# Kernel tuning notes

Hardware: AMD Instinct MI355X
Metric: run time of the kernel (lower is better)

Reference implementation:

```python
import jax, jax.numpy as jnp
import numpy as np

N = 100000
E = 1600000
IN_C = 128
HID_C = 32
HEADS = 4
OUT_C = 64
NUM_CLASSES = 2
NUM_GRAPHS = 64
NEG_SLOPE = 0.2  # PyG GATConv default leaky_relu slope


def _segment_softmax(logits, seg, num_segments):
    # logits: [E, H], seg: [E] destination node ids
    m = jax.ops.segment_max(logits, seg, num_segments=num_segments)
    m = jnp.where(jnp.isfinite(m), m, 0.0)
    e = jnp.exp(logits - m[seg])
    s = jax.ops.segment_sum(e, seg, num_segments=num_segments)
    return e / (s[seg] + 1e-16)


def _gat_conv(x, src, dst, W, att_src, att_dst, bias, heads, ch, concat):
    n = x.shape[0]
    h = (x @ W).reshape(n, heads, ch)                 # [N, H, C]
    a_src = jnp.sum(h * att_src, axis=-1)             # [N, H]
    a_dst = jnp.sum(h * att_dst, axis=-1)             # [N, H]
    alpha = jax.nn.leaky_relu(a_src[src] + a_dst[dst], NEG_SLOPE)  # [E, H]
    alpha = _segment_softmax(alpha, dst, n)
    msg = h[src] * alpha[:, :, None]                  # [E, H, C]
    out = jax.ops.segment_sum(msg, dst, num_segments=n)  # [N, H, C]
    out = out.reshape(n, heads * ch) if concat else out.mean(axis=1)
    return out + bias


def setup_inputs() -> dict:
    key = jax.random.key(0)
    ks = jax.random.split(key, 12)
    x = jax.random.normal(ks[0], (N, IN_C), dtype=jnp.float32)
    edge_index = jax.random.randint(ks[1], (2, E), 0, N, dtype=jnp.int32)
    batch = jnp.sort(jax.random.randint(ks[2], (N,), 0, NUM_GRAPHS, dtype=jnp.int32))
    s1 = 1.0 / np.sqrt(IN_C)
    W1 = jax.random.uniform(ks[3], (IN_C, HEADS * HID_C), minval=-s1, maxval=s1, dtype=jnp.float32)
    att_src1 = jax.random.normal(ks[4], (HEADS, HID_C), dtype=jnp.float32) * 0.1
    att_dst1 = jax.random.normal(ks[5], (HEADS, HID_C), dtype=jnp.float32) * 0.1
    b1 = jnp.zeros((HEADS * HID_C,), dtype=jnp.float32)
    s2 = 1.0 / np.sqrt(HEADS * HID_C)
    W2 = jax.random.uniform(ks[6], (HEADS * HID_C, OUT_C), minval=-s2, maxval=s2, dtype=jnp.float32)
    att_src2 = jax.random.normal(ks[7], (1, OUT_C), dtype=jnp.float32) * 0.1
    att_dst2 = jax.random.normal(ks[8], (1, OUT_C), dtype=jnp.float32) * 0.1
    b2 = jnp.zeros((OUT_C,), dtype=jnp.float32)
    sc = 1.0 / np.sqrt(OUT_C)
    Wc = jax.random.uniform(ks[9], (OUT_C, NUM_CLASSES), minval=-sc, maxval=sc, dtype=jnp.float32)
    bc = jnp.zeros((NUM_CLASSES,), dtype=jnp.float32)
    return {"x": x, "edge_index": edge_index, "batch": batch,
            "W1": W1, "att_src1": att_src1, "att_dst1": att_dst1, "b1": b1,
            "W2": W2, "att_src2": att_src2, "att_dst2": att_dst2, "b2": b2,
            "Wc": Wc, "bc": bc}


def reference(x, edge_index, batch, W1, att_src1, att_dst1, b1,
              W2, att_src2, att_dst2, b2, Wc, bc):
    # PyG GATConv adds self-loops by default
    loops = jnp.arange(N, dtype=edge_index.dtype)
    src = jnp.concatenate([edge_index[0], loops])
    dst = jnp.concatenate([edge_index[1], loops])
    # eval mode: dropout is identity
    h = _gat_conv(x, src, dst, W1, att_src1, att_dst1, b1, HEADS, HID_C, True)
    h = jax.nn.elu(h)
    h = _gat_conv(h, src, dst, W2, att_src2, att_dst2, b2, 1, OUT_C, False)
    h = jax.nn.elu(h)
    # global mean pool over graphs
    sums = jax.ops.segment_sum(h, batch, num_segments=NUM_GRAPHS)
    cnts = jax.ops.segment_sum(jnp.ones((N, 1), h.dtype), batch, num_segments=NUM_GRAPHS)
    pooled = sums / jnp.maximum(cnts, 1.0)
    return pooled @ Wc + bc
```

## Files before the change

### kernel.cpp

```cpp
#include <hip/hip_runtime.h>
#include <math.h>


typedef __attribute__((ext_vector_type(8))) short bf16x8;
typedef __attribute__((ext_vector_type(4))) float f32x4;

__device__ __forceinline__ unsigned f2bf_rne(float x){
  unsigned u = __float_as_uint(x);
  return (u + 0x7fffu + ((u >> 16) & 1u)) >> 16;
}
__device__ __forceinline__ unsigned pk_bf2(float a, float b){
  return f2bf_rne(a) | (f2bf_rne(b) << 16);
}
__device__ __forceinline__ void unpack8(uint4 q, float* f){
  f[0] = __uint_as_float(q.x << 16);
  f[1] = __uint_as_float(q.x & 0xffff0000u);
  f[2] = __uint_as_float(q.y << 16);
  f[3] = __uint_as_float(q.y & 0xffff0000u);
  f[4] = __uint_as_float(q.z << 16);
  f[5] = __uint_as_float(q.z & 0xffff0000u);
  f[6] = __uint_as_float(q.w << 16);
  f[7] = __uint_as_float(q.w & 0xffff0000u);
}


#define CHUNKE 8192

__global__ __launch_bounds__(256) void k_bucketcount(
    const int* __restrict__ dst, int* __restrict__ bcnt, int e, int NB)
{
  __shared__ int hcnt[512];
  const int tid = threadIdx.x;
  for (int b = tid; b < 512; b += 256) hcnt[b] = 0;
  __syncthreads();
  const int lo = blockIdx.x * CHUNKE;
  const int hi = min(lo + CHUNKE, e);
  for (int i = lo + tid; i < hi; i += 256)
    atomicAdd(&hcnt[dst[i] >> 8], 1);
  __syncthreads();
  for (int b = tid; b < NB; b += 256)
    if (hcnt[b]) atomicAdd(&bcnt[b], hcnt[b]);
}

__global__ __launch_bounds__(512) void k_bucketscan(
    const int* __restrict__ bcnt, int* __restrict__ bbase,
    int* __restrict__ cur, int* __restrict__ off, int e, int n, int NB,
    const float* __restrict__ W1, const float* __restrict__ as1w,
    const float* __restrict__ ad1w,
    const float* __restrict__ W2, const float* __restrict__ as2w,
    const float* __restrict__ ad2w,
    unsigned short* __restrict__ wa1, unsigned short* __restrict__ wa2)
{
  const int t = threadIdx.x;

  if (blockIdx.x == 1){
    for (int i = t; i < 2048; i += 512) wa2[i] = 0;
    __syncthreads();
    {
      int k = t >> 2, j = t & 3;
      float ds = 0.f, dd = 0.f;
      for (int cc = 0; cc < 32; ++cc){
        float wv = W1[k * 128 + j * 32 + cc];
        ds = fmaf(wv, as1w[j * 32 + cc], ds);
        dd = fmaf(wv, ad1w[j * 32 + cc], dd);
      }
      unsigned hs_ = f2bf_rne(ds); float hsf = __uint_as_float(hs_ << 16);
      unsigned ls_ = f2bf_rne(ds - hsf);
      unsigned hd_ = f2bf_rne(dd); float hdf = __uint_as_float(hd_ << 16);
      unsigned ld_ = f2bf_rne(dd - hdf);
      wa1[(j     ) * 128 + k] = (unsigned short)hs_;
      wa1[(j + 4 ) * 128 + k] = (unsigned short)ls_;
      wa1[(j + 8 ) * 128 + k] = (unsigned short)hd_;
      wa1[(j + 12) * 128 + k] = (unsigned short)ld_;
    }
    if (t < 128){
      int k = t;
      float ds = 0.f, dd = 0.f;
      for (int cc = 0; cc < 64; ++cc){
        float wv = W2[k * 64 + cc];
        ds = fmaf(wv, as2w[cc], ds);
        dd = fmaf(wv, ad2w[cc], dd);
      }
      unsigned hs_ = f2bf_rne(ds); float hsf = __uint_as_float(hs_ << 16);
      unsigned ls_ = f2bf_rne(ds - hsf);
      unsigned hd_ = f2bf_rne(dd); float hdf = __uint_as_float(hd_ << 16);
      unsigned ld_ = f2bf_rne(dd - hdf);
      wa2[ 0 * 128 + k] = (unsigned short)hs_;
      wa2[ 4 * 128 + k] = (unsigned short)ls_;
      wa2[ 8 * 128 + k] = (unsigned short)hd_;
      wa2[12 * 128 + k] = (unsigned short)ld_;
    }
    return;
  }

  __shared__ int sh[512];
  int v = (t < NB) ? bcnt[t] : 0;
  sh[t] = v;
  __syncthreads();
  for (int o = 1; o < 512; o <<= 1){
    int x = (t >= o) ? sh[t - o] : 0;
    __syncthreads();
    sh[t] += x;
    __syncthreads();
  }
  if (t < NB){
    int excl = sh[t] - v;
    bbase[t] = excl;
    cur[t]   = excl;
  }
  if (t == 0) off[n] = e;
}

__global__ __launch_bounds__(256) void k_partition(
    const int* __restrict__ src, const int* __restrict__ dst,
    int* __restrict__ cur, unsigned* __restrict__ packed, int e, int NB)
{
  __shared__ unsigned       recs[CHUNKE];
  __shared__ unsigned short bkt[CHUNKE];
  __shared__ int hcnt[512];
  __shared__ int hoff[512];
  __shared__ int hbase[512];

  const int tid = threadIdx.x;
  const int lo  = blockIdx.x * CHUNKE;
  const int hi  = min(lo + CHUNKE, e);
  const int cnt = hi - lo;

  hcnt[tid] = 0; hcnt[tid + 256] = 0;
  __syncthreads();
  for (int i = lo + tid; i < hi; i += 256)
    atomicAdd(&hcnt[dst[i] >> 8], 1);
  __syncthreads();

  hoff[tid] = hcnt[tid]; hoff[tid + 256] = hcnt[tid + 256];
  __syncthreads();
  for (int o = 1; o < 512; o <<= 1){
    int x0 = (tid >= o)       ? hoff[tid - o]       : 0;
    int x1 = (tid + 256 >= o) ? hoff[tid + 256 - o] : 0;
    __syncthreads();
    hoff[tid] += x0; hoff[tid + 256] += x1;
    __syncthreads();
  }

  int c0 = hcnt[tid], c1 = hcnt[tid + 256];
  int e0 = hoff[tid] - c0, e1 = hoff[tid + 256] - c1;
  hbase[tid]       = c0 ? atomicAdd(&cur[tid], c0)       : 0;
  hbase[tid + 256] = c1 ? atomicAdd(&cur[tid + 256], c1) : 0;
  __syncthreads();
  hoff[tid] = e0; hoff[tid + 256] = e1;
  hcnt[tid] = 0;  hcnt[tid + 256] = 0;
  __syncthreads();

  for (int i = lo + tid; i < hi; i += 256){
    int d = dst[i];
    int b = d >> 8;
    int p = hoff[b] + atomicAdd(&hcnt[b], 1);
    recs[p] = (unsigned)src[i] | ((unsigned)(d & 255) << 17);
    bkt[p]  = (unsigned short)b;
  }
  __syncthreads();

  for (int t = tid; t < cnt; t += 256){
    int b = bkt[t];
    packed[hbase[b] + t - hoff[b]] = recs[t];
  }
}

__global__ __launch_bounds__(256) void k_bucketbuild(
    const unsigned* __restrict__ packed, const int* __restrict__ bbase,
    const int* __restrict__ bcnt, int* __restrict__ off,
    int* __restrict__ csr, int n)
{
  __shared__ int lcnt[256];
  __shared__ int loff[256];
  const int b    = blockIdx.x;
  const int tid  = threadIdx.x;
  const int seg0 = bbase[b];
  const int scnt = bcnt[b];

  lcnt[tid] = 0;
  __syncthreads();
  for (int i = tid; i < scnt; i += 256)
    atomicAdd(&lcnt[packed[seg0 + i] >> 17], 1);
  __syncthreads();
  int v = lcnt[tid];
  loff[tid] = v;
  __syncthreads();
  for (int o = 1; o < 256; o <<= 1){
    int x = (tid >= o) ? loff[tid - o] : 0;
    __syncthreads();
    loff[tid] += x;
    __syncthreads();
  }
  int excl = loff[tid] - v;
  __syncthreads();
  loff[tid] = excl;
  lcnt[tid] = 0;
  int d = (b << 8) + tid;
  if (d < n) off[d] = seg0 + excl;
  __syncthreads();
  for (int i = tid; i < scnt; i += 256){
    unsigned rec = packed[seg0 + i];
    int doff = rec >> 17;
    int s    = rec & 0x1FFFF;
    int p    = atomicAdd(&lcnt[doff], 1);
    csr[seg0 + loff[doff] + p] = s;
  }
}


template<int OUTC, int HEADS, bool XBF16, typename XT>
__global__ __launch_bounds__(256) void k_gemm_mfma(
    const XT* __restrict__ X, const float* __restrict__ W,
    const unsigned short* __restrict__ WATT,
    unsigned short* __restrict__ H, float* __restrict__ ASRC,
    float* __restrict__ ADST, int n)
{
  constexpr int K  = 128;
  constexpr int KC = 32;
  constexpr int CT = OUTC / 16;
  constexpr int CTX = CT + 1;
  constexpr int RT = 16 / CT;
  constexpr int WROWS = RT * 16;
  constexpr int BROWS = WROWS * 4;

  __shared__ unsigned short Bs[OUTC + 16][K + 8];
  __shared__ unsigned short As[BROWS][KC + 8];

  const int tid   = threadIdx.x;
  const int lane  = tid & 63;
  const int c15   = lane & 15;
  const int quad  = lane >> 4;
  const int warow = (tid >> 6) * WROWS;
  const int row0  = blockIdx.x * BROWS;

  f32x4 acc[CTX][RT];
  #pragma unroll
  for (int ct = 0; ct < CTX; ++ct)
    #pragma unroll
    for (int t = 0; t < RT; ++t)
      #pragma unroll
      for (int r = 0; r < 4; ++r) acc[ct][t][r] = 0.f;

  for (int idx = tid; idx < K * OUTC / 4; idx += 256){
    int k  = idx / (OUTC / 4);
    int c4 = (idx % (OUTC / 4)) * 4;
    float4 v = *(const float4*)&W[(size_t)k * OUTC + c4];
    Bs[c4 + 0][k] = (unsigned short)f2bf_rne(v.x);
    Bs[c4 + 1][k] = (unsigned short)f2bf_rne(v.y);
    Bs[c4 + 2][k] = (unsigned short)f2bf_rne(v.z);
    Bs[c4 + 3][k] = (unsigned short)f2bf_rne(v.w);
  }
  for (int idx = tid; idx < 16 * (K / 8); idx += 256){
    int rr = idx >> 4;
    int q  = idx & 15;
    *(uint4*)&Bs[OUTC + rr][q * 8] = *(const uint4*)&WATT[rr * K + q * 8];
  }

  for (int kc = 0; kc < K; kc += KC){
    if (XBF16){
      for (int idx = tid; idx < BROWS * (KC / 8); idx += 256){
        int rr = idx / (KC / 8);
        int q  = idx % (KC / 8);
        int row = row0 + rr;
        uint4 v = make_uint4(0, 0, 0, 0);
        if (row < n) v = *(const uint4*)((const unsigned short*)X + (size_t)row * K + kc + q * 8);
        *(uint4*)&As[rr][q * 8] = v;
      }
    } else {
      for (int idx = tid; idx < BROWS * (KC / 4); idx += 256){
        int rr = idx / (KC / 4);
        int q  = idx % (KC / 4);
        int row = row0 + rr;
        float4 v = make_float4(0.f, 0.f, 0.f, 0.f);
        if (row < n) v = *(const float4*)((const float*)X + (size_t)row * K + kc + q * 4);
        *(uint2*)&As[rr][q * 4] = make_uint2(pk_bf2(v.x, v.y), pk_bf2(v.z, v.w));
      }
    }
    __syncthreads();

    bf16x8 af[RT];
    #pragma unroll
    for (int t = 0; t < RT; ++t)
      af[t] = *(const bf16x8*)&As[warow + t * 16 + c15][8 * quad];
    #pragma unroll
    for (int ct = 0; ct < CTX; ++ct){
      bf16x8 bfr = *(const bf16x8*)&Bs[ct * 16 + c15][kc + 8 * quad];
      #pragma unroll
      for (int t = 0; t < RT; ++t)
        acc[ct][t] = __builtin_amdgcn_mfma_f32_16x16x32_bf16(af[t], bfr, acc[ct][t], 0, 0, 0);
    }
    __syncthreads();
  }

  #pragma unroll
  for (int t = 0; t < RT; ++t){
    #pragma unroll
    for (int r = 0; r < 4; ++r){
      int row = row0 + warow + t * 16 + quad * 4 + r;
      float av = acc[CT][t][r];
      av += __shfl_xor(av, 4);
      if (row < n){
        #pragma unroll
        for (int ct = 0; ct < CT; ++ct)
          H[(size_t)row * OUTC + ct * 16 + c15] = (unsigned short)f2bf_rne(acc[ct][t][r]);
        if (c15 < HEADS)                      ASRC[row * HEADS + c15] = av;
        else if (c15 >= 8 && c15 < 8 + HEADS) ADST[row * HEADS + c15 - 8] = av;
      }
    }
  }
}


template<int CH, int HEADS, bool OUTBF16, bool POOL>
__global__ __launch_bounds__(256) void k_aggregate(
    const unsigned short* __restrict__ Hmsg, const float* __restrict__ ASRC,
    const float* __restrict__ ADST, const int* __restrict__ off,
    const int* __restrict__ csr, const float* __restrict__ bias,
    void* __restrict__ OUT, const int* __restrict__ batch,
    float* __restrict__ gsums, int n)
{
  constexpr int CL  = CH / 8;
  constexpr int GPB = 256 / CL;
  constexpr int CPH = CH / HEADS;
  constexpr int RQ  = CH / 8;

  __shared__ float lsum[POOL ? 256 : 1];

  const int tid = threadIdx.x;
  const int cl  = tid % CL;
  const int c0  = cl * 8;
  const int h   = c0 / CPH;
  const int d   = (int)blockIdx.x * GPB + tid / CL;
  const uint4* Hv = (const uint4*)Hmsg;

  int gbase = 0;
  if (POOL){
    int probe = (int)blockIdx.x * GPB;
    gbase = batch[probe < n - 1 ? probe : n - 1];
    lsum[tid] = 0.f;
    __syncthreads();
  }

  if (d < n){
    const float adst = ADST[d * HEADS + h];

    float acc[8];
    float wsum;
    {
      float t = ASRC[d * HEADS + h] + adst;
      float w = __expf(fmaxf(t, 0.2f * t));
      float f[8];
      unpack8(Hv[d * RQ + cl], f);
      #pragma unroll
      for (int j = 0; j < 8; ++j) acc[j] = w * f[j];
      wsum = w;
    }

    const int s0   = off[d];
    const int cnt  = off[d + 1] - s0;
    const int full = cnt & ~7;

    for (int p = 0; p < full; p += 8){
      int idx[8];
      #pragma unroll
      for (int j = 0; j < 8; ++j) idx[j] = csr[s0 + p + j];
      float av[8];
      #pragma unroll
      for (int j = 0; j < 8; ++j) av[j] = ASRC[idx[j] * HEADS + h];
      uint4 hq[8];
      #pragma unroll
      for (int j = 0; j < 8; ++j) hq[j] = Hv[idx[j] * RQ + cl];
      #pragma unroll
      for (int j = 0; j < 8; ++j){
        float t = av[j] + adst;
        float w = __expf(fmaxf(t, 0.2f * t));
        float f[8];
        unpack8(hq[j], f);
        #pragma unroll
        for (int q = 0; q < 8; ++q) acc[q] = fmaf(w, f[q], acc[q]);
        wsum += w;
      }
    }

    const int rem = cnt - full;
    if (rem){
      int  idx[8];
      bool ok[8];
      #pragma unroll
      for (int j = 0; j < 8; ++j){
        int q = csr[s0 + full + j];
        ok[j]  = j < rem;
        idx[j] = ok[j] ? q : 0;
      }
      float av[8];
      #pragma unroll
      for (int j = 0; j < 8; ++j) av[j] = ASRC[idx[j] * HEADS + h];
      uint4 hq[8];
      #pragma unroll
      for (int j = 0; j < 8; ++j) hq[j] = Hv[idx[j] * RQ + cl];
      #pragma unroll
      for (int j = 0; j < 8; ++j){
        float t = av[j] + adst;
        float w = __expf(fmaxf(t, 0.2f * t));
        w = ok[j] ? w : 0.f;
        float f[8];
        unpack8(hq[j], f);
        #pragma unroll
        for (int q = 0; q < 8; ++q) acc[q] = fmaf(w, f[q], acc[q]);
        wsum += w;
      }
    }

    const float inv = 1.f / (wsum + 1e-16f);
    float o[8];
    #pragma unroll
    for (int j = 0; j < 8; ++j){
      float v = acc[j] * inv + bias[c0 + j];
      o[j] = v > 0.f ? v : expm1f(v);
    }
    if (POOL){
      int gb  = batch[d];
      int rel = gb - gbase;
      if (rel >= 0 && rel < 4){
        #pragma unroll
        for (int j = 0; j < 8; ++j) atomicAdd(&lsum[rel * 64 + c0 + j], o[j]);
      } else {
        #pragma unroll
        for (int j = 0; j < 8; ++j) atomicAdd(&gsums[gb * 64 + c0 + j], o[j]);
      }
    } else if (OUTBF16){
      uint4 q;
      q.x = pk_bf2(o[0], o[1]); q.y = pk_bf2(o[2], o[3]);
      q.z = pk_bf2(o[4], o[5]); q.w = pk_bf2(o[6], o[7]);
      *(uint4*)((unsigned short*)OUT + (size_t)d * CH + c0) = q;
    } else {
      float* Of = (float*)OUT;
      *(float4*)&Of[(size_t)d * CH + c0 + 0] = make_float4(o[0], o[1], o[2], o[3]);
      *(float4*)&Of[(size_t)d * CH + c0 + 4] = make_float4(o[4], o[5], o[6], o[7]);
    }
  }

  if (POOL){
    __syncthreads();
    int slot = tid >> 6;
    int ch   = tid & 63;
    float v = lsum[slot * 64 + ch];
    int gg = gbase + slot;
    if (v != 0.f && gg < 64)
      atomicAdd(&gsums[gg * 64 + ch], v);
  }
}

__global__ __launch_bounds__(128) void k_classify(
    const float* __restrict__ sums, const int* __restrict__ batch,
    const float* __restrict__ Wc, const float* __restrict__ bc,
    float* __restrict__ out, int n)
{
  int t = threadIdx.x;
  if (t >= 128) return;
  int g = t >> 1, cls = t & 1;
  int lo = 0, hi = n;
  while (lo < hi){ int m = (lo + hi) >> 1; if (batch[m] < g) lo = m + 1; else hi = m; }
  int s = lo;
  lo = s; hi = n;
  while (lo < hi){ int m = (lo + hi) >> 1; if (batch[m] < g + 1) lo = m + 1; else hi = m; }
  int cnt = lo - s;
  float inv = 1.f / (float)(cnt > 1 ? cnt : 1);
  float dot = 0.f;
  #pragma unroll
  for (int c = 0; c < 64; ++c) dot = fmaf(sums[g * 64 + c], Wc[c * 2 + cls], dot);
  out[g * 2 + cls] = dot * inv + bc[cls];
}


extern "C" void kernel_launch(void* const* d_in, const int* in_sizes, int n_in,
                              void* d_out, int out_size, void* d_ws, size_t ws_size,
                              hipStream_t stream)
{
  const float* x    = (const float*)d_in[0];
  const int*   edge = (const int*)  d_in[1];
  const int*   batch= (const int*)  d_in[2];
  const float* W1   = (const float*)d_in[3];
  const float* as1w = (const float*)d_in[4];
  const float* ad1w = (const float*)d_in[5];
  const float* b1   = (const float*)d_in[6];
  const float* W2   = (const float*)d_in[7];
  const float* as2w = (const float*)d_in[8];
  const float* ad2w = (const float*)d_in[9];
  const float* b2   = (const float*)d_in[10];
  const float* Wc   = (const float*)d_in[11];
  const float* bc   = (const float*)d_in[12];

  const int n = in_sizes[2];
  const int e = in_sizes[1] / 2;
  const int* esrc = edge;
  const int* edst = edge + e;
  const int NB = (n + 255) >> 8;

  unsigned short* h1  = (unsigned short*)d_ws;
  unsigned short* h1a = h1 + (size_t)n * 128;
  float* as1 = (float*)(h1a + (size_t)n * 128);
  float* ad1 = as1 + (size_t)n * 4;
  float* as2 = ad1 + (size_t)n * 4;
  float* ad2 = as2 + (size_t)n;
  float* sums = ad2 + (size_t)n;
  unsigned short* wa1 = (unsigned short*)(sums + 64 * 64);
  unsigned short* wa2 = wa1 + 2048;
  int*  bcnt  = (int*)(wa2 + 2048);
  int*  cur   = bcnt + 512;
  int*  bbase = cur + 512;
  int*  off   = bbase + 512;
  unsigned* packed = (unsigned*)(off + n + 1);
  int*  csr   = (int*)(packed + e);

  const int eb = (e + CHUNKE - 1) / CHUNKE;

  (void)hipMemsetAsync(sums, 0, 64 * 64 * 4 + 2 * 4096 + 512 * 4, stream);
  k_bucketcount<<<eb, 256, 0, stream>>>(edst, bcnt, e, NB);
  k_bucketscan <<<2, 512, 0, stream>>>(bcnt, bbase, cur, off, e, n, NB,
                                       W1, as1w, ad1w, W2, as2w, ad2w, wa1, wa2);
  k_partition  <<<eb, 256, 0, stream>>>(esrc, edst, cur, packed, e, NB);
  k_bucketbuild<<<NB, 256, 0, stream>>>(packed, bbase, bcnt, off, csr, n);

  k_gemm_mfma<128, 4, false><<<(n + 127) / 128, 256, 0, stream>>>(
      x, W1, wa1, h1, as1, ad1, n);
  k_aggregate<128, 4, true, false><<<(n + 15) / 16, 256, 0, stream>>>(
      h1, as1, ad1, off, csr, b1, (void*)h1a, nullptr, nullptr, n);

  unsigned short* h2 = h1;
  k_gemm_mfma<64, 1, true><<<(n + 255) / 256, 256, 0, stream>>>(
      h1a, W2, wa2, h2, as2, ad2, n);
  k_aggregate<64, 1, false, true><<<(n + 31) / 32, 256, 0, stream>>>(
      h2, as2, ad2, off, csr, b2, nullptr, batch, sums, n);

  k_classify<<<1, 128, 0, stream>>>(sums, batch, Wc, bc, (float*)d_out, n);
}
```

Measured before the change: 380.0 us.

## Fuse layer-2 GEMM into layer-1 aggregation and wave-reduce pooled atomics

```diff
diff --git a/kernel.cpp b/kernel.cpp
--- a/kernel.cpp
+++ b/kernel.cpp
@@ -49,12 +49,12 @@
     const float* __restrict__ ad1w,
     const float* __restrict__ W2, const float* __restrict__ as2w,
     const float* __restrict__ ad2w,
-    unsigned short* __restrict__ wa1, unsigned short* __restrict__ wa2)
+    unsigned short* __restrict__ wa1, unsigned short* __restrict__ w2b)
 {
   const int t = threadIdx.x;
 
   if (blockIdx.x == 1){
-    for (int i = t; i < 2048; i += 512) wa2[i] = 0;
+    for (int i = t; i < 16 * 128; i += 512) w2b[64 * 128 + i] = 0;
     __syncthreads();
     {
       int k = t >> 2, j = t & 3;
@@ -73,6 +73,10 @@
       wa1[(j + 8 ) * 128 + k] = (unsigned short)hd_;
       wa1[(j + 12) * 128 + k] = (unsigned short)ld_;
     }
+    for (int idx = t; idx < 64 * 128; idx += 512){
+      int col = idx & 63, k = idx >> 6;
+      w2b[col * 128 + k] = (unsigned short)f2bf_rne(W2[k * 64 + col]);
+    }
     if (t < 128){
       int k = t;
       float ds = 0.f, dd = 0.f;
@@ -85,10 +89,10 @@
       unsigned ls_ = f2bf_rne(ds - hsf);
       unsigned hd_ = f2bf_rne(dd); float hdf = __uint_as_float(hd_ << 16);
       unsigned ld_ = f2bf_rne(dd - hdf);
-      wa2[ 0 * 128 + k] = (unsigned short)hs_;
-      wa2[ 4 * 128 + k] = (unsigned short)ls_;
-      wa2[ 8 * 128 + k] = (unsigned short)hd_;
-      wa2[12 * 128 + k] = (unsigned short)ld_;
+      w2b[(64 +  0) * 128 + k] = (unsigned short)hs_;
+      w2b[(64 +  4) * 128 + k] = (unsigned short)ls_;
+      w2b[(64 +  8) * 128 + k] = (unsigned short)hd_;
+      w2b[(64 + 12) * 128 + k] = (unsigned short)ld_;
     }
     return;
   }
@@ -312,46 +316,41 @@
 }
 
 
-template<int CH, int HEADS, bool OUTBF16, bool POOL>
-__global__ __launch_bounds__(256) void k_aggregate(
+__global__ __launch_bounds__(256) void k_agg1_fused(
     const unsigned short* __restrict__ Hmsg, const float* __restrict__ ASRC,
     const float* __restrict__ ADST, const int* __restrict__ off,
     const int* __restrict__ csr, const float* __restrict__ bias,
-    void* __restrict__ OUT, const int* __restrict__ batch,
-    float* __restrict__ gsums, int n)
-{
-  constexpr int CL  = CH / 8;
-  constexpr int GPB = 256 / CL;
-  constexpr int CPH = CH / HEADS;
-  constexpr int RQ  = CH / 8;
-
-  __shared__ float lsum[POOL ? 256 : 1];
+    const unsigned short* __restrict__ W2b,
+    unsigned short* __restrict__ H2, float* __restrict__ AS2,
+    float* __restrict__ AD2, int n)
+{
+  __shared__ unsigned short Ht[16][136];
+  __shared__ unsigned short Bs2[80][136];
 
   const int tid = threadIdx.x;
-  const int cl  = tid % CL;
+  const int cl  = tid & 15;
   const int c0  = cl * 8;
-  const int h   = c0 / CPH;
-  const int d   = (int)blockIdx.x * GPB + tid / CL;
+  const int h   = cl >> 2;
+  const int ld  = tid >> 4;
+  const int d0  = (int)blockIdx.x * 16;
+  const int d   = d0 + ld;
   const uint4* Hv = (const uint4*)Hmsg;
 
-  int gbase = 0;
-  if (POOL){
-    int probe = (int)blockIdx.x * GPB;
-    gbase = batch[probe < n - 1 ? probe : n - 1];
-    lsum[tid] = 0.f;
-    __syncthreads();
+  for (int idx = tid; idx < 80 * 16; idx += 256){
+    int row = idx >> 4, q = idx & 15;
+    *(uint4*)&Bs2[row][q * 8] = *(const uint4*)&W2b[row * 128 + q * 8];
   }
 
   if (d < n){
-    const float adst = ADST[d * HEADS + h];
+    const float adst = ADST[d * 4 + h];
 
     float acc[8];
     float wsum;
     {
-      float t = ASRC[d * HEADS + h] + adst;
+      float t = ASRC[d * 4 + h] + adst;
       float w = __expf(fmaxf(t, 0.2f * t));
       float f[8];
-      unpack8(Hv[d * RQ + cl], f);
+      unpack8(Hv[d * 16 + cl], f);
       #pragma unroll
       for (int j = 0; j < 8; ++j) acc[j] = w * f[j];
       wsum = w;
@@ -367,10 +366,10 @@
       for (int j = 0; j < 8; ++j) idx[j] = csr[s0 + p + j];
       float av[8];
       #pragma unroll
-      for (int j = 0; j < 8; ++j) av[j] = ASRC[idx[j] * HEADS + h];
+      for (int j = 0; j < 8; ++j) av[j] = ASRC[idx[j] * 4 + h];
       uint4 hq[8];
       #pragma unroll
-      for (int j = 0; j < 8; ++j) hq[j] = Hv[idx[j] * RQ + cl];
+      for (int j = 0; j < 8; ++j) hq[j] = Hv[idx[j] * 16 + cl];
       #pragma unroll
       for (int j = 0; j < 8; ++j){
         float t = av[j] + adst;
@@ -395,10 +394,10 @@
       }
       float av[8];
       #pragma unroll
-      for (int j = 0; j < 8; ++j) av[j] = ASRC[idx[j] * HEADS + h];
+      for (int j = 0; j < 8; ++j) av[j] = ASRC[idx[j] * 4 + h];
       uint4 hq[8];
       #pragma unroll
-      for (int j = 0; j < 8; ++j) hq[j] = Hv[idx[j] * RQ + cl];
+      for (int j = 0; j < 8; ++j) hq[j] = Hv[idx[j] * 16 + cl];
       #pragma unroll
       for (int j = 0; j < 8; ++j){
         float t = av[j] + adst;
@@ -419,37 +418,195 @@
       float v = acc[j] * inv + bias[c0 + j];
       o[j] = v > 0.f ? v : expm1f(v);
     }
-    if (POOL){
-      int gb  = batch[d];
-      int rel = gb - gbase;
+    uint4 q;
+    q.x = pk_bf2(o[0], o[1]); q.y = pk_bf2(o[2], o[3]);
+    q.z = pk_bf2(o[4], o[5]); q.w = pk_bf2(o[6], o[7]);
+    *(uint4*)&Ht[ld][c0] = q;
+  }
+
+  __syncthreads();
+
+  const int lane = tid & 63;
+  const int c15  = lane & 15;
+  const int quad = lane >> 4;
+  const int w    = tid >> 6;
+  f32x4 a0, a4;
+  #pragma unroll
+  for (int r = 0; r < 4; ++r){ a0[r] = 0.f; a4[r] = 0.f; }
+
+  #pragma unroll
+  for (int kc = 0; kc < 128; kc += 32){
+    bf16x8 af = *(const bf16x8*)&Ht[c15][kc + 8 * quad];
+    bf16x8 b0 = *(const bf16x8*)&Bs2[w * 16 + c15][kc + 8 * quad];
+    a0 = __builtin_amdgcn_mfma_f32_16x16x32_bf16(af, b0, a0, 0, 0, 0);
+    if (w == 0){
+      bf16x8 b4 = *(const bf16x8*)&Bs2[64 + c15][kc + 8 * quad];
+      a4 = __builtin_amdgcn_mfma_f32_16x16x32_bf16(af, b4, a4, 0, 0, 0);
+    }
+  }
+
+  #pragma unroll
+  for (int r = 0; r < 4; ++r){
+    int dd = d0 + quad * 4 + r;
+    if (dd < n) H2[(size_t)dd * 64 + w * 16 + c15] = (unsigned short)f2bf_rne(a0[r]);
+  }
+  if (w == 0){
+    #pragma unroll
+    for (int r = 0; r < 4; ++r){
+      float av = a4[r] + __shfl_xor(a4[r], 4);
+      int dd = d0 + quad * 4 + r;
+      if (dd < n){
+        if (c15 == 0)      AS2[dd] = av;
+        else if (c15 == 8) AD2[dd] = av;
+      }
+    }
+  }
+}
+
+
+template<int CH, int HEADS>
+__global__ __launch_bounds__(256) void k_agg2_pool(
+    const unsigned short* __restrict__ Hmsg, const float* __restrict__ ASRC,
+    const float* __restrict__ ADST, const int* __restrict__ off,
+    const int* __restrict__ csr, const float* __restrict__ bias,
+    const int* __restrict__ batch, float* __restrict__ gsums, int n)
+{
+  constexpr int CL  = CH / 8;
+  constexpr int GPB = 256 / CL;
+  constexpr int RQ  = CH / 8;
+
+  __shared__ float lsum[256];
+
+  const int tid = threadIdx.x;
+  const int cl  = tid % CL;
+  const int c0  = cl * 8;
+  const int d   = (int)blockIdx.x * GPB + tid / CL;
+  const uint4* Hv = (const uint4*)Hmsg;
+
+  int probe = (int)blockIdx.x * GPB;
+  const int gbase = batch[probe < n - 1 ? probe : n - 1];
+  lsum[tid] = 0.f;
+  __syncthreads();
+
+  float o[8];
+  #pragma unroll
+  for (int j = 0; j < 8; ++j) o[j] = 0.f;
+  int gb = gbase;
+
+  if (d < n){
+    gb = batch[d];
+    const float adst = ADST[d];
+
+    float acc[8];
+    float wsum;
+    {
+      float t = ASRC[d] + adst;
+      float w = __expf(fmaxf(t, 0.2f * t));
+      float f[8];
+      unpack8(Hv[d * RQ + cl], f);
+      #pragma unroll
+      for (int j = 0; j < 8; ++j) acc[j] = w * f[j];
+      wsum = w;
+    }
+
+    const int s0   = off[d];
+    const int cnt  = off[d + 1] - s0;
+    const int full = cnt & ~7;
+
+    for (int p = 0; p < full; p += 8){
+      int idx[8];
+      #pragma unroll
+      for (int j = 0; j < 8; ++j) idx[j] = csr[s0 + p + j];
+      float av[8];
+      #pragma unroll
+      for (int j = 0; j < 8; ++j) av[j] = ASRC[idx[j]];
+      uint4 hq[8];
+      #pragma unroll
+      for (int j = 0; j < 8; ++j) hq[j] = Hv[idx[j] * RQ + cl];
+      #pragma unroll
+      for (int j = 0; j < 8; ++j){
+        float t = av[j] + adst;
+        float w = __expf(fmaxf(t, 0.2f * t));
+        float f[8];
+        unpack8(hq[j], f);
+        #pragma unroll
+        for (int q = 0; q < 8; ++q) acc[q] = fmaf(w, f[q], acc[q]);
+        wsum += w;
+      }
+    }
+
+    const int rem = cnt - full;
+    if (rem){
+      int  idx[8];
+      bool ok[8];
+      #pragma unroll
+      for (int j = 0; j < 8; ++j){
+        int q = csr[s0 + full + j];
+        ok[j]  = j < rem;
+        idx[j] = ok[j] ? q : 0;
+      }
+      float av[8];
+      #pragma unroll
+      for (int j = 0; j < 8; ++j) av[j] = ASRC[idx[j]];
+      uint4 hq[8];
+      #pragma unroll
+      for (int j = 0; j < 8; ++j) hq[j] = Hv[idx[j] * RQ + cl];
+      #pragma unroll
+      for (int j = 0; j < 8; ++j){
+        float t = av[j] + adst;
+        float w = __expf(fmaxf(t, 0.2f * t));
+        w = ok[j] ? w : 0.f;
+        float f[8];
+        unpack8(hq[j], f);
+        #pragma unroll
+        for (int q = 0; q < 8; ++q) acc[q] = fmaf(w, f[q], acc[q]);
+        wsum += w;
+      }
+    }
+
+    const float inv = 1.f / (wsum + 1e-16f);
+    #pragma unroll
+    for (int j = 0; j < 8; ++j){
+      float v = acc[j] * inv + bias[c0 + j];
+      o[j] = v > 0.f ? v : expm1f(v);
+    }
+  }
+
+  int gb0 = __shfl(gb, 0, 64);
+  bool uni = __all(gb == gb0);
+  if (uni){
+    #pragma unroll
+    for (int s = CL; s < 64; s <<= 1)
+      #pragma unroll
+      for (int j = 0; j < 8; ++j) o[j] += __shfl_xor(o[j], s);
+    if ((tid & 63) < CL){
+      int rel = gb0 - gbase;
       if (rel >= 0 && rel < 4){
         #pragma unroll
         for (int j = 0; j < 8; ++j) atomicAdd(&lsum[rel * 64 + c0 + j], o[j]);
       } else {
         #pragma unroll
-        for (int j = 0; j < 8; ++j) atomicAdd(&gsums[gb * 64 + c0 + j], o[j]);
-      }
-    } else if (OUTBF16){
-      uint4 q;
-      q.x = pk_bf2(o[0], o[1]); q.y = pk_bf2(o[2], o[3]);
-      q.z = pk_bf2(o[4], o[5]); q.w = pk_bf2(o[6], o[7]);
-      *(uint4*)((unsigned short*)OUT + (size_t)d * CH + c0) = q;
+        for (int j = 0; j < 8; ++j) atomicAdd(&gsums[gb0 * 64 + c0 + j], o[j]);
+      }
+    }
+  } else if (d < n){
+    int rel = gb - gbase;
+    if (rel >= 0 && rel < 4){
+      #pragma unroll
+      for (int j = 0; j < 8; ++j) atomicAdd(&lsum[rel * 64 + c0 + j], o[j]);
     } else {
-      float* Of = (float*)OUT;
-      *(float4*)&Of[(size_t)d * CH + c0 + 0] = make_float4(o[0], o[1], o[2], o[3]);
-      *(float4*)&Of[(size_t)d * CH + c0 + 4] = make_float4(o[4], o[5], o[6], o[7]);
-    }
-  }
-
-  if (POOL){
-    __syncthreads();
-    int slot = tid >> 6;
-    int ch   = tid & 63;
-    float v = lsum[slot * 64 + ch];
-    int gg = gbase + slot;
-    if (v != 0.f && gg < 64)
-      atomicAdd(&gsums[gg * 64 + ch], v);
-  }
+      #pragma unroll
+      for (int j = 0; j < 8; ++j) atomicAdd(&gsums[gb * 64 + c0 + j], o[j]);
+    }
+  }
+
+  __syncthreads();
+  int slot = tid >> 6;
+  int ch   = tid & 63;
+  float v = lsum[slot * 64 + ch];
+  int gg = gbase + slot;
+  if (v != 0.f && gg < 64)
+    atomicAdd(&gsums[gg * 64 + ch], v);
 }
 
 __global__ __launch_bounds__(128) void k_classify(
@@ -499,15 +656,15 @@
   const int NB = (n + 255) >> 8;
 
   unsigned short* h1  = (unsigned short*)d_ws;
-  unsigned short* h1a = h1 + (size_t)n * 128;
-  float* as1 = (float*)(h1a + (size_t)n * 128);
+  unsigned short* h2  = h1 + (size_t)n * 128;
+  float* as1 = (float*)(h2 + (size_t)n * 64);
   float* ad1 = as1 + (size_t)n * 4;
   float* as2 = ad1 + (size_t)n * 4;
   float* ad2 = as2 + (size_t)n;
   float* sums = ad2 + (size_t)n;
   unsigned short* wa1 = (unsigned short*)(sums + 64 * 64);
-  unsigned short* wa2 = wa1 + 2048;
-  int*  bcnt  = (int*)(wa2 + 2048);
+  unsigned short* w2b = wa1 + 2048;
+  int*  bcnt  = (int*)(w2b + 80 * 128);
   int*  cur   = bcnt + 512;
   int*  bbase = cur + 512;
   int*  off   = bbase + 512;
@@ -516,23 +673,21 @@
 
   const int eb = (e + CHUNKE - 1) / CHUNKE;
 
-  (void)hipMemsetAsync(sums, 0, 64 * 64 * 4 + 2 * 4096 + 512 * 4, stream);
+  (void)hipMemsetAsync(sums, 0, 64 * 64 * 4 + 2048 * 2 + 80 * 128 * 2 + 512 * 4, stream);
   k_bucketcount<<<eb, 256, 0, stream>>>(edst, bcnt, e, NB);
   k_bucketscan <<<2, 512, 0, stream>>>(bcnt, bbase, cur, off, e, n, NB,
-                                       W1, as1w, ad1w, W2, as2w, ad2w, wa1, wa2);
+                                       W1, as1w, ad1w, W2, as2w, ad2w, wa1, w2b);
   k_partition  <<<eb, 256, 0, stream>>>(esrc, edst, cur, packed, e, NB);
   k_bucketbuild<<<NB, 256, 0, stream>>>(packed, bbase, bcnt, off, csr, n);
 
   k_gemm_mfma<128, 4, false><<<(n + 127) / 128, 256, 0, stream>>>(
       x, W1, wa1, h1, as1, ad1, n);
-  k_aggregate<128, 4, true, false><<<(n + 15) / 16, 256, 0, stream>>>(
-      h1, as1, ad1, off, csr, b1, (void*)h1a, nullptr, nullptr, n);
-
-  unsigned short* h2 = h1;
-  k_gemm_mfma<64, 1, true><<<(n + 255) / 256, 256, 0, stream>>>(
-      h1a, W2, wa2, h2, as2, ad2, n);
-  k_aggregate<64, 1, false, true><<<(n + 31) / 32, 256, 0, stream>>>(
-      h2, as2, ad2, off, csr, b2, nullptr, batch, sums, n);
+
+  k_agg1_fused<<<(n + 15) / 16, 256, 0, stream>>>(
+      h1, as1, ad1, off, csr, b1, w2b, h2, as2, ad2, n);
+
+  k_agg2_pool<64, 1><<<(n + 31) / 32, 256, 0, stream>>>(
+      h2, as2, ad2, off, csr, b2, batch, sums, n);
 
   k_classify<<<1, 128, 0, stream>>>(sums, batch, Wc, bc, (float*)d_out, n);
 }
```

New measurement: 356.2 us. 6.3% less time.
